# Kernel optimization log

Measured on AMD Instinct MI355X. Metric: run time of the kernel, lower is better.

Reference implementation:

```python
import jax, jax.numpy as jnp
import numpy as np

N_NODES = 100000
N_EDGES = 1600000
INPUT_DIM, HIDDEN_DIM, OUTPUT_DIM = 128, 256, 2
BN_EPS = 1e-5


def setup_inputs() -> dict:
    key = jax.random.key(0)
    ks = jax.random.split(key, 8)
    x = jax.random.normal(ks[0], (N_NODES, INPUT_DIM), jnp.float32)
    edge_index = jax.random.randint(ks[1], (2, N_EDGES), 0, N_NODES, dtype=jnp.int32).astype(jnp.int64)
    # Glorot-ish init for GCNConv weights; PyG GCNConv has bias by default.
    def glorot(k, fan_in, fan_out):
        s = jnp.sqrt(6.0 / (fan_in + fan_out))
        return jax.random.uniform(k, (fan_in, fan_out), jnp.float32, -s, s)
    return {
        "x": x,
        "edge_index": edge_index,
        "W0": glorot(ks[2], INPUT_DIM, HIDDEN_DIM),
        "b0": jnp.zeros((HIDDEN_DIM,), jnp.float32),
        "W1": glorot(ks[3], HIDDEN_DIM, HIDDEN_DIM),
        "b1": jnp.zeros((HIDDEN_DIM,), jnp.float32),
        "W2": glorot(ks[4], HIDDEN_DIM, OUTPUT_DIM),
        "b2": jnp.zeros((OUTPUT_DIM,), jnp.float32),
        "gamma0": jnp.ones((HIDDEN_DIM,), jnp.float32),
        "beta0": jnp.zeros((HIDDEN_DIM,), jnp.float32),
        "gamma1": jnp.ones((HIDDEN_DIM,), jnp.float32),
        "beta1": jnp.zeros((HIDDEN_DIM,), jnp.float32),
    }


def _gcn_norm(edge_index, num_nodes):
    # PyG gcn_norm: add self-loops, deg over destination, D^-1/2 A_hat D^-1/2
    loop = jnp.arange(num_nodes, dtype=edge_index.dtype)
    src = jnp.concatenate([edge_index[0], loop])
    dst = jnp.concatenate([edge_index[1], loop])
    deg = jax.ops.segment_sum(jnp.ones_like(dst, jnp.float32), dst, num_segments=num_nodes)
    dinv = jax.lax.rsqrt(jnp.maximum(deg, 1.0))  # deg >= 1 due to self-loops
    norm = dinv[src] * dinv[dst]  # [E + N]
    return src, dst, norm


def _gcn_conv(x, W, b, src, dst, norm, num_nodes):
    h = x @ W                          # [N, out] dense GEMM first (PyG order)
    msg = h[src] * norm[:, None]       # gather + edge scale
    out = jax.ops.segment_sum(msg, dst, num_segments=num_nodes)  # scatter-add
    return out + b


def _batchnorm(x, gamma, beta):
    # training-mode BatchNorm1d over nodes (biased variance, as torch uses for normalization)
    mean = jnp.mean(x, axis=0)
    var = jnp.mean(jnp.square(x - mean), axis=0)
    return (x - mean) * jax.lax.rsqrt(var + BN_EPS) * gamma + beta


def reference(x, edge_index, W0, b0, W1, b1, W2, b2, gamma0, beta0, gamma1, beta1):
    n = x.shape[0]
    src, dst, norm = _gcn_norm(edge_index, n)
    h = _gcn_conv(x, W0, b0, src, dst, norm, n)
    h = jax.nn.relu(_batchnorm(h, gamma0, beta0))  # dropout is identity (eval / deterministic)
    h = _gcn_conv(h, W1, b1, src, dst, norm, n)
    h = jax.nn.relu(_batchnorm(h, gamma1, beta1))
    out = _gcn_conv(h, W2, b2, src, dst, norm, n)
    return out
```

## Files before the change

### kernel.cpp

```cpp
#include <hip/hip_runtime.h>
#include <hip/hip_fp16.h>


#define BN_EPS 1e-5f

union HF4 { float4 f; __half2 h[4]; };

typedef __attribute__((ext_vector_type(8))) _Float16 f16x8;
typedef __attribute__((ext_vector_type(4))) float f32x4;

__global__ void detect_i64(const unsigned int* __restrict__ w, int* flag) {
  __shared__ unsigned int red[256];
  unsigned int v = 0;
  int t = threadIdx.x;
  for (int i = t; i < 1024; i += 256) v |= w[2 * i + 1];
  red[t] = v;
  __syncthreads();
  for (int s = 128; s > 0; s >>= 1) {
    if (t < s) red[t] |= red[t + s];
    __syncthreads();
  }
  if (t == 0) *flag = (red[0] == 0u) ? 1 : 0;
}

__global__ void convert_deg(const unsigned int* __restrict__ w, const int* __restrict__ flag,
                            int* __restrict__ srcI, int* __restrict__ dstI,
                            int* __restrict__ deg, int E) {
  int i = blockIdx.x * blockDim.x + threadIdx.x;
  if (i >= E) return;
  int f = *flag;
  int s = (int)(f ? w[2 * (size_t)i] : w[i]);
  int d = (int)(f ? w[2 * ((size_t)E + i)] : w[(size_t)E + i]);
  srcI[i] = s;
  dstI[i] = d;
  atomicAdd(&deg[d], 1);
}

__global__ void make_dinv(const int* __restrict__ deg, float* __restrict__ dinv,
                          float* __restrict__ stats, int N) {
  int i = blockIdx.x * blockDim.x + threadIdx.x;
  if (i < 512) stats[i] = 0.f;
  if (i < N) dinv[i] = rsqrtf((float)deg[i] + 1.0f);
}

__global__ void scan_partial(const int* __restrict__ deg, int* __restrict__ blksum, int N) {
  __shared__ int s[256];
  int b = blockIdx.x, t = threadIdx.x;
  int base = b * 1024 + t * 4;
  int v = 0;
#pragma unroll
  for (int k = 0; k < 4; ++k) {
    int i = base + k;
    if (i < N) v += deg[i];
  }
  s[t] = v;
  __syncthreads();
  for (int st = 128; st > 0; st >>= 1) {
    if (t < st) s[t] += s[t + st];
    __syncthreads();
  }
  if (t == 0) blksum[b] = s[0];
}

__global__ void scan_blk(int* __restrict__ blksum, int B) {
  __shared__ int s[256];
  int t = threadIdx.x;
  int v = (t < B) ? blksum[t] : 0;
  s[t] = v;
  __syncthreads();
  for (int off = 1; off < 256; off <<= 1) {
    int u = (t >= off) ? s[t - off] : 0;
    __syncthreads();
    s[t] += u;
    __syncthreads();
  }
  if (t < B) blksum[t] = s[t] - v;
}

__global__ void scan_final(const int* __restrict__ deg, const int* __restrict__ blkoff,
                           int* __restrict__ rowptr, int* __restrict__ fill, int N, int E) {
  __shared__ int s[256];
  int b = blockIdx.x, t = threadIdx.x;
  int base = b * 1024 + t * 4;
  int v[4];
  int sum = 0;
#pragma unroll
  for (int k = 0; k < 4; ++k) {
    int i = base + k;
    v[k] = (i < N) ? deg[i] : 0;
    sum += v[k];
  }
  s[t] = sum;
  __syncthreads();
  for (int off = 1; off < 256; off <<= 1) {
    int u = (t >= off) ? s[t - off] : 0;
    __syncthreads();
    s[t] += u;
    __syncthreads();
  }
  int ex = s[t] - sum + blkoff[b];
#pragma unroll
  for (int k = 0; k < 4; ++k) {
    int i = base + k;
    if (i < N) {
      rowptr[i] = ex;
      fill[i] = ex;
      ex += v[k];
    }
  }
  if (b == 0 && t == 0) rowptr[N] = E;
}

__global__ void csr_scatter(const int* __restrict__ src, const int* __restrict__ dst,
                            const float* __restrict__ dinv, int* __restrict__ fill,
                            int2* __restrict__ edge, int E) {
  int e = blockIdx.x * blockDim.x + threadIdx.x;
  if (e >= E) return;
  int s = src[e], d = dst[e];
  int slot = atomicAdd(&fill[d], 1);
  edge[slot] = make_int2(s, __float_as_int(dinv[s] * dinv[d]));
}

__global__ void f32_to_f16(const float4* __restrict__ in, float4* __restrict__ outh, long n8) {
  long t = (long)blockIdx.x * blockDim.x + threadIdx.x;
  if (t >= n8) return;
  float4 a = in[2 * t], b = in[2 * t + 1];
  HF4 o;
  o.h[0] = __floats2half2_rn(a.x, a.y);
  o.h[1] = __floats2half2_rn(a.z, a.w);
  o.h[2] = __floats2half2_rn(b.x, b.y);
  o.h[3] = __floats2half2_rn(b.z, b.w);
  outh[t] = o.f;
}

__global__ void pack_w2(const float* __restrict__ W0, const float* __restrict__ W1,
                        _Float16* __restrict__ W0p, _Float16* __restrict__ W1p) {
  int idx = blockIdx.x * blockDim.x + threadIdx.x;
  const float* W = (idx < 128 * 256) ? W0 : W1;
  _Float16* Wp = (idx < 128 * 256) ? W0p : W1p;
  int li = (idx < 128 * 256) ? idx : idx - 128 * 256;
  int k = li >> 8, n = li & 255;
  int kb = k >> 5, kk = k & 31, seg = kk >> 3, j = kk & 7;
  Wp[(((kb * 4 + seg) * 256) + n) * 8 + j] = (_Float16)W[li];
}

template <int LPN, bool BN>
__global__ void agg_gather_h(const float4* __restrict__ inh, float4* __restrict__ outh,
                             const int* __restrict__ rowptr, const int2* __restrict__ edge,
                             const float* __restrict__ dinv,
                             const float* __restrict__ scale, const float* __restrict__ shift,
                             int N) {
  long g = (long)blockIdx.x * blockDim.x + threadIdx.x;
  int n = (int)(g / LPN);
  int lane = (int)(g & (LPN - 1));
  if (n >= N) return;
  float sc[8], sh[8];
  if (BN) {
    int c0 = lane * 8;
#pragma unroll
    for (int i = 0; i < 8; ++i) {
      sc[i] = scale[c0 + i];
      sh[i] = shift[c0 + i];
    }
  }
  auto xf = [&](const HF4& u, float* o) {
#pragma unroll
    for (int i = 0; i < 4; ++i) {
      float2 f = __half22float2(u.h[i]);
      o[2 * i] = f.x;
      o[2 * i + 1] = f.y;
    }
    if (BN) {
#pragma unroll
      for (int i = 0; i < 8; ++i) o[i] = fmaxf(o[i] * sc[i] + sh[i], 0.f);
    }
  };
  float ws = dinv[n];
  ws *= ws;
  float acc[8], v[8];
  {
    HF4 u;
    u.f = inh[(long)n * LPN + lane];
    xf(u, v);
#pragma unroll
    for (int i = 0; i < 8; ++i) acc[i] = ws * v[i];
  }
  int beg = rowptr[n], end = rowptr[n + 1];
  int j = beg;
  for (; j + 3 < end; j += 4) {
    int2 e0 = edge[j], e1 = edge[j + 1], e2 = edge[j + 2], e3 = edge[j + 3];
    float w0 = __int_as_float(e0.y), w1 = __int_as_float(e1.y);
    float w2 = __int_as_float(e2.y), w3 = __int_as_float(e3.y);
    HF4 a, b, c, d;
    a.f = inh[(long)e0.x * LPN + lane];
    b.f = inh[(long)e1.x * LPN + lane];
    c.f = inh[(long)e2.x * LPN + lane];
    d.f = inh[(long)e3.x * LPN + lane];
    float va[8], vb[8], vc[8], vd[8];
    xf(a, va); xf(b, vb); xf(c, vc); xf(d, vd);
#pragma unroll
    for (int i = 0; i < 8; ++i)
      acc[i] += w0 * va[i] + w1 * vb[i] + w2 * vc[i] + w3 * vd[i];
  }
  for (; j < end; ++j) {
    int2 e0 = edge[j];
    float w0 = __int_as_float(e0.y);
    HF4 a;
    a.f = inh[(long)e0.x * LPN + lane];
    float va[8];
    xf(a, va);
#pragma unroll
    for (int i = 0; i < 8; ++i) acc[i] += w0 * va[i];
  }
  HF4 o;
  o.h[0] = __floats2half2_rn(acc[0], acc[1]);
  o.h[1] = __floats2half2_rn(acc[2], acc[3]);
  o.h[2] = __floats2half2_rn(acc[4], acc[5]);
  o.h[3] = __floats2half2_rn(acc[6], acc[7]);
  outh[(long)n * LPN + lane] = o.f;
}

template <int K, int NC>
__global__ __launch_bounds__(256) void gemm_mfma(const _Float16* __restrict__ A,
                                                 const float4* __restrict__ Wpack,
                                                 _Float16* __restrict__ H,
                                                 float* __restrict__ gsum,
                                                 float* __restrict__ gsq, int M) {
  __shared__ float red0[NC];
  __shared__ float red1[NC];
  int tid = threadIdx.x;
  if (tid < NC) {
    red0[tid] = 0.f;
    red1[tid] = 0.f;
  }
  __syncthreads();
  int wave = tid >> 6;
  int lane = tid & 63;
  int row0 = (blockIdx.x * 4 + wave) * 32;
  bool active = row0 + 31 < M;
  int arow0 = active ? row0 : 0;
  int r = lane & 15;
  int seg = lane >> 4;
  f32x4 acc0[NC / 16], acc1[NC / 16];
#pragma unroll
  for (int t = 0; t < NC / 16; ++t) {
    acc0[t] = (f32x4){0.f, 0.f, 0.f, 0.f};
    acc1[t] = (f32x4){0.f, 0.f, 0.f, 0.f};
  }
  const _Float16* arowA = A + (long)(arow0 + r) * K;
  const _Float16* arowB = A + (long)(arow0 + 16 + r) * K;
#pragma unroll
  for (int k0 = 0; k0 < K; k0 += 32) {
    f16x8 af0 = *(const f16x8*)(arowA + k0 + seg * 8);
    f16x8 af1 = *(const f16x8*)(arowB + k0 + seg * 8);
    const float4* wp = Wpack + ((k0 >> 5) * 4 + seg) * NC;
#pragma unroll
    for (int t = 0; t < NC / 16; ++t) {
      f16x8 bf = *(const f16x8*)(wp + t * 16 + r);
      acc0[t] = __builtin_amdgcn_mfma_f32_16x16x32_f16(af0, bf, acc0[t], 0, 0, 0);
      acc1[t] = __builtin_amdgcn_mfma_f32_16x16x32_f16(af1, bf, acc1[t], 0, 0, 0);
    }
  }
#pragma unroll
  for (int t = 0; t < NC / 16; ++t) {
    int c = t * 16 + r;
    float s = 0.f, q = 0.f;
#pragma unroll
    for (int qq = 0; qq < 4; ++qq) {
      float v0 = acc0[t][qq], v1 = acc1[t][qq];
      s += v0 + v1;
      q += v0 * v0 + v1 * v1;
    }
    s += __shfl_xor(s, 16, 64);
    s += __shfl_xor(s, 32, 64);
    q += __shfl_xor(q, 16, 64);
    q += __shfl_xor(q, 32, 64);
    if (active) {
      if (seg == 0) {
        atomicAdd(&red0[c], s);
        atomicAdd(&red1[c], q);
      }
#pragma unroll
      for (int qq = 0; qq < 4; ++qq) {
        H[(long)(row0 + seg * 4 + qq) * NC + c] = (_Float16)acc0[t][qq];
        H[(long)(row0 + 16 + seg * 4 + qq) * NC + c] = (_Float16)acc1[t][qq];
      }
    }
  }
  __syncthreads();
  if (tid < NC) {
    atomicAdd(&gsum[tid], red0[tid]);
    atomicAdd(&gsq[tid], red1[tid]);
  }
}

__global__ void bn_finalize(float* __restrict__ gsum, float* __restrict__ gsq,
                            const float* __restrict__ gamma, const float* __restrict__ beta,
                            float* __restrict__ scale, float* __restrict__ shift, float invN) {
  int c = threadIdx.x;
  float mean = gsum[c] * invN;
  float var = fmaxf(gsq[c] * invN - mean * mean, 0.f);
  float sc = rsqrtf(var + BN_EPS) * gamma[c];
  scale[c] = sc;
  shift[c] = beta[c] - mean * sc;
  gsum[c] = 0.f;
  gsq[c] = 0.f;
}

__global__ void bn_apply_proj(const float4* __restrict__ h_in, const float* __restrict__ scale,
                              const float* __restrict__ shift, const float* __restrict__ W2,
                              float* __restrict__ P, int N) {
  int tid = threadIdx.x;
  int row = blockIdx.x * 8 + (tid >> 5);
  int lr = tid & 31;
  if (row >= N) return;
  HF4 u;
  u.f = h_in[(long)row * 32 + lr];
  int c0 = lr * 8;
  float s0 = 0.f, s1 = 0.f;
#pragma unroll
  for (int i = 0; i < 4; ++i) {
    float2 f = __half22float2(u.h[i]);
    int ca = c0 + 2 * i, cb = c0 + 2 * i + 1;
    float va = fmaxf(f.x * scale[ca] + shift[ca], 0.f);
    float vb = fmaxf(f.y * scale[cb] + shift[cb], 0.f);
    s0 += va * W2[2 * ca] + vb * W2[2 * cb];
    s1 += va * W2[2 * ca + 1] + vb * W2[2 * cb + 1];
  }
#pragma unroll
  for (int off = 16; off > 0; off >>= 1) {
    s0 += __shfl_down(s0, off, 32);
    s1 += __shfl_down(s1, off, 32);
  }
  if (lr == 0) {
    P[2 * row] = s0;
    P[2 * row + 1] = s1;
  }
}

__global__ void final_gather(const float* __restrict__ P, float* __restrict__ out,
                             const int* __restrict__ rowptr, const int2* __restrict__ edge,
                             const float* __restrict__ dinv, const float* __restrict__ b2,
                             int N) {
  int n = blockIdx.x * blockDim.x + threadIdx.x;
  if (n >= N) return;
  float w = dinv[n] * dinv[n];
  float a0 = w * P[2 * n + 0];
  float a1 = w * P[2 * n + 1];
  int end = rowptr[n + 1];
  for (int j = rowptr[n]; j < end; ++j) {
    int2 e = edge[j];
    float ww = __int_as_float(e.y);
    a0 += ww * P[2 * e.x + 0];
    a1 += ww * P[2 * e.x + 1];
  }
  out[2 * n + 0] = a0 + b2[0];
  out[2 * n + 1] = a1 + b2[1];
}

extern "C" void kernel_launch(void* const* d_in, const int* in_sizes, int n_in,
                              void* d_out, int out_size, void* d_ws, size_t ws_size,
                              hipStream_t stream) {
  const float* x = (const float*)d_in[0];
  const unsigned int* eidx = (const unsigned int*)d_in[1];
  const float* W0 = (const float*)d_in[2];
  const float* W1 = (const float*)d_in[4];
  const float* W2 = (const float*)d_in[6];
  const float* b2 = (const float*)d_in[7];
  const float* gamma0 = (const float*)d_in[8];
  const float* beta0 = (const float*)d_in[9];
  const float* gamma1 = (const float*)d_in[10];
  const float* beta1 = (const float*)d_in[11];

  const int N = in_sizes[0] / 128;
  const int E = in_sizes[1] / 2;
  float* out = (float*)d_out;

  char* base = (char*)d_ws;
  size_t off = 0;
  auto alloc = [&](size_t bytes) {
    size_t o = off;
    off = (off + bytes + 255) & ~(size_t)255;
    return o;
  };
  const size_t o_edge = alloc((size_t)E * 8);
  const size_t o_rowptr = alloc((size_t)(N + 1) * 4);
  const size_t o_deg = alloc((size_t)N * 4);
  const size_t o_fill = alloc((size_t)N * 4);
  const size_t o_dinv = alloc((size_t)N * 4);
  const size_t o_blk = alloc(1024 * 4);
  const size_t o_flag = alloc(256);
  const size_t o_stats = alloc(4096);
  const size_t o_P = alloc((size_t)N * 2 * 4);
  const size_t o_W0p = alloc(128 * 256 * 2);
  const size_t o_W1p = alloc(256 * 256 * 2);
  const size_t o_H1 = alloc((size_t)N * 256 * 2);
  const size_t o_H2 = alloc((size_t)N * 256 * 2);

  int2* edge = (int2*)(base + o_edge);
  int* rowptr = (int*)(base + o_rowptr);
  int* deg = (int*)(base + o_deg);
  int* fill = (int*)(base + o_fill);
  float* dinv = (float*)(base + o_dinv);
  int* blk = (int*)(base + o_blk);
  int* flag = (int*)(base + o_flag);
  float* gsum = (float*)(base + o_stats);
  float* gsq = gsum + 256;
  float* scale = gsum + 512;
  float* shift = gsum + 768;
  float* P = (float*)(base + o_P);
  _Float16* W0p = (_Float16*)(base + o_W0p);
  _Float16* W1p = (_Float16*)(base + o_W1p);
  float4* H1 = (float4*)(base + o_H1);
  float4* H2 = (float4*)(base + o_H2);
  int* idx32 = (int*)(base + o_H2);
  int* srcI = idx32;
  int* dstI = idx32 + E;

  auto cdiv = [](long a, long b) { return (int)((a + b - 1) / b); };
  const float invN = 1.0f / (float)N;
  const int B1 = cdiv(N, 1024);

  hipLaunchKernelGGL(detect_i64, dim3(1), dim3(256), 0, stream, eidx, flag);
  hipMemsetAsync(deg, 0, (size_t)N * 4, stream);
  hipLaunchKernelGGL(convert_deg, dim3(cdiv(E, 256)), dim3(256), 0, stream, eidx, flag, srcI,
                     dstI, deg, E);

  hipLaunchKernelGGL(make_dinv, dim3(cdiv(N, 256)), dim3(256), 0, stream, deg, dinv, gsum, N);
  hipLaunchKernelGGL(scan_partial, dim3(B1), dim3(256), 0, stream, deg, blk, N);
  hipLaunchKernelGGL(scan_blk, dim3(1), dim3(256), 0, stream, blk, B1);
  hipLaunchKernelGGL(scan_final, dim3(B1), dim3(256), 0, stream, deg, blk, rowptr, fill, N, E);
  hipLaunchKernelGGL(csr_scatter, dim3(cdiv(E, 256)), dim3(256), 0, stream, srcI, dstI, dinv,
                     fill, edge, E);
  hipLaunchKernelGGL(pack_w2, dim3(cdiv(384 * 256, 256)), dim3(256), 0, stream, W0, W1, W0p, W1p);
  hipLaunchKernelGGL(f32_to_f16, dim3(cdiv((long)N * 16, 256)), dim3(256), 0, stream,
                     (const float4*)x, H1, (long)N * 16);

  hipLaunchKernelGGL((agg_gather_h<16, false>), dim3(cdiv((long)N * 16, 256)), dim3(256), 0,
                     stream, H1, H2, rowptr, edge, dinv, nullptr, nullptr, N);
  hipLaunchKernelGGL((gemm_mfma<128, 256>), dim3(cdiv(N, 128)), dim3(256), 0, stream,
                     (const _Float16*)H2, (const float4*)W0p, (_Float16*)H1, gsum, gsq, N);

  hipLaunchKernelGGL(bn_finalize, dim3(1), dim3(256), 0, stream, gsum, gsq, gamma0, beta0, scale,
                     shift, invN);

  hipLaunchKernelGGL((agg_gather_h<32, true>), dim3(cdiv((long)N * 32, 256)), dim3(256), 0,
                     stream, H1, H2, rowptr, edge, dinv, scale, shift, N);
  hipLaunchKernelGGL((gemm_mfma<256, 256>), dim3(cdiv(N, 128)), dim3(256), 0, stream,
                     (const _Float16*)H2, (const float4*)W1p, (_Float16*)H1, gsum, gsq, N);

  hipLaunchKernelGGL(bn_finalize, dim3(1), dim3(256), 0, stream, gsum, gsq, gamma1, beta1, scale,
                     shift, invN);
  hipLaunchKernelGGL(bn_apply_proj, dim3(cdiv(N, 8)), dim3(256), 0, stream, (const float4*)H1,
                     scale, shift, W2, P, N);

  hipLaunchKernelGGL(final_gather, dim3(cdiv(N, 256)), dim3(256), 0, stream, P, out, rowptr,
                     edge, dinv, b2, N);
}
```

Before: 554.1 us.

## Store CSR column indices only, recompute edge weights from dinv; fuse prep kernels

After: 603.4 us. 8.9% more time.

```diff
diff --git a/kernel.cpp b/kernel.cpp
--- a/kernel.cpp
+++ b/kernel.cpp
@@ -27,31 +27,53 @@
                             int* __restrict__ srcI, int* __restrict__ dstI,
                             int* __restrict__ deg, int E) {
   int i = blockIdx.x * blockDim.x + threadIdx.x;
-  if (i >= E) return;
+  int e0 = 2 * i;
+  if (e0 >= E) return;
   int f = *flag;
-  int s = (int)(f ? w[2 * (size_t)i] : w[i]);
-  int d = (int)(f ? w[2 * ((size_t)E + i)] : w[(size_t)E + i]);
-  srcI[i] = s;
-  dstI[i] = d;
-  atomicAdd(&deg[d], 1);
-}
-
-__global__ void make_dinv(const int* __restrict__ deg, float* __restrict__ dinv,
-                          float* __restrict__ stats, int N) {
-  int i = blockIdx.x * blockDim.x + threadIdx.x;
-  if (i < 512) stats[i] = 0.f;
-  if (i < N) dinv[i] = rsqrtf((float)deg[i] + 1.0f);
-}
-
-__global__ void scan_partial(const int* __restrict__ deg, int* __restrict__ blksum, int N) {
+  if (e0 + 1 < E) {
+    int s0, s1, d0, d1;
+    if (f) {
+      uint4 sv = ((const uint4*)w)[i];
+      uint4 dv = ((const uint4*)(w + 2 * (size_t)E))[i];
+      s0 = (int)sv.x; s1 = (int)sv.z;
+      d0 = (int)dv.x; d1 = (int)dv.z;
+    } else {
+      int2 sv = ((const int2*)w)[i];
+      int2 dv = ((const int2*)(w + (size_t)E))[i];
+      s0 = sv.x; s1 = sv.y;
+      d0 = dv.x; d1 = dv.y;
+    }
+    *(int2*)(srcI + e0) = make_int2(s0, s1);
+    *(int2*)(dstI + e0) = make_int2(d0, d1);
+    atomicAdd(&deg[d0], 1);
+    atomicAdd(&deg[d1], 1);
+  } else {
+    int s = (int)(f ? w[2 * (size_t)e0] : w[e0]);
+    int d = (int)(f ? w[2 * ((size_t)E + e0)] : w[(size_t)E + e0]);
+    srcI[e0] = s;
+    dstI[e0] = d;
+    atomicAdd(&deg[d], 1);
+  }
+}
+
+__global__ void scan_partial(const int* __restrict__ deg, int* __restrict__ blksum,
+                             float* __restrict__ dinv, float* __restrict__ stats, int N) {
   __shared__ int s[256];
   int b = blockIdx.x, t = threadIdx.x;
+  if (b == 0) {
+    stats[t] = 0.f;
+    stats[t + 256] = 0.f;
+  }
   int base = b * 1024 + t * 4;
   int v = 0;
 #pragma unroll
   for (int k = 0; k < 4; ++k) {
     int i = base + k;
-    if (i < N) v += deg[i];
+    if (i < N) {
+      int dg = deg[i];
+      v += dg;
+      dinv[i] = rsqrtf((float)dg + 1.0f);
+    }
   }
   s[t] = v;
   __syncthreads();
@@ -112,41 +134,43 @@
 }
 
 __global__ void csr_scatter(const int* __restrict__ src, const int* __restrict__ dst,
-                            const float* __restrict__ dinv, int* __restrict__ fill,
-                            int2* __restrict__ edge, int E) {
+                            int* __restrict__ fill, int* __restrict__ col, int E) {
   int e = blockIdx.x * blockDim.x + threadIdx.x;
   if (e >= E) return;
   int s = src[e], d = dst[e];
   int slot = atomicAdd(&fill[d], 1);
-  edge[slot] = make_int2(s, __float_as_int(dinv[s] * dinv[d]));
-}
-
-__global__ void f32_to_f16(const float4* __restrict__ in, float4* __restrict__ outh, long n8) {
-  long t = (long)blockIdx.x * blockDim.x + threadIdx.x;
-  if (t >= n8) return;
-  float4 a = in[2 * t], b = in[2 * t + 1];
-  HF4 o;
-  o.h[0] = __floats2half2_rn(a.x, a.y);
-  o.h[1] = __floats2half2_rn(a.z, a.w);
-  o.h[2] = __floats2half2_rn(b.x, b.y);
-  o.h[3] = __floats2half2_rn(b.z, b.w);
-  outh[t] = o.f;
-}
-
-__global__ void pack_w2(const float* __restrict__ W0, const float* __restrict__ W1,
-                        _Float16* __restrict__ W0p, _Float16* __restrict__ W1p) {
-  int idx = blockIdx.x * blockDim.x + threadIdx.x;
-  const float* W = (idx < 128 * 256) ? W0 : W1;
-  _Float16* Wp = (idx < 128 * 256) ? W0p : W1p;
-  int li = (idx < 128 * 256) ? idx : idx - 128 * 256;
-  int k = li >> 8, n = li & 255;
-  int kb = k >> 5, kk = k & 31, seg = kk >> 3, j = kk & 7;
-  Wp[(((kb * 4 + seg) * 256) + n) * 8 + j] = (_Float16)W[li];
+  col[slot] = s;
+}
+
+__global__ void prep_pack_convert(const float* __restrict__ W0, const float* __restrict__ W1,
+                                  _Float16* __restrict__ W0p, _Float16* __restrict__ W1p,
+                                  const float4* __restrict__ x, float4* __restrict__ xh,
+                                  long n8) {
+  long b = blockIdx.x;
+  if (b < 384) {
+    int idx = (int)b * 256 + threadIdx.x;
+    const float* W = (idx < 128 * 256) ? W0 : W1;
+    _Float16* Wp = (idx < 128 * 256) ? W0p : W1p;
+    int li = (idx < 128 * 256) ? idx : idx - 128 * 256;
+    int k = li >> 8, n = li & 255;
+    int kb = k >> 5, kk = k & 31, seg = kk >> 3, j = kk & 7;
+    Wp[(((kb * 4 + seg) * 256) + n) * 8 + j] = (_Float16)W[li];
+  } else {
+    long t = (b - 384) * 256 + threadIdx.x;
+    if (t >= n8) return;
+    float4 a = x[2 * t], c = x[2 * t + 1];
+    HF4 o;
+    o.h[0] = __floats2half2_rn(a.x, a.y);
+    o.h[1] = __floats2half2_rn(a.z, a.w);
+    o.h[2] = __floats2half2_rn(c.x, c.y);
+    o.h[3] = __floats2half2_rn(c.z, c.w);
+    xh[t] = o.f;
+  }
 }
 
 template <int LPN, bool BN>
 __global__ void agg_gather_h(const float4* __restrict__ inh, float4* __restrict__ outh,
-                             const int* __restrict__ rowptr, const int2* __restrict__ edge,
+                             const int* __restrict__ rowptr, const int* __restrict__ col,
                              const float* __restrict__ dinv,
                              const float* __restrict__ scale, const float* __restrict__ shift,
                              int N) {
@@ -175,8 +199,8 @@
       for (int i = 0; i < 8; ++i) o[i] = fmaxf(o[i] * sc[i] + sh[i], 0.f);
     }
   };
-  float ws = dinv[n];
-  ws *= ws;
+  float dn = dinv[n];
+  float ws = dn * dn;
   float acc[8], v[8];
   {
     HF4 u;
@@ -188,14 +212,14 @@
   int beg = rowptr[n], end = rowptr[n + 1];
   int j = beg;
   for (; j + 3 < end; j += 4) {
-    int2 e0 = edge[j], e1 = edge[j + 1], e2 = edge[j + 2], e3 = edge[j + 3];
-    float w0 = __int_as_float(e0.y), w1 = __int_as_float(e1.y);
-    float w2 = __int_as_float(e2.y), w3 = __int_as_float(e3.y);
+    int c0 = col[j], c1 = col[j + 1], c2 = col[j + 2], c3 = col[j + 3];
+    float w0 = dinv[c0] * dn, w1 = dinv[c1] * dn;
+    float w2 = dinv[c2] * dn, w3 = dinv[c3] * dn;
     HF4 a, b, c, d;
-    a.f = inh[(long)e0.x * LPN + lane];
-    b.f = inh[(long)e1.x * LPN + lane];
-    c.f = inh[(long)e2.x * LPN + lane];
-    d.f = inh[(long)e3.x * LPN + lane];
+    a.f = inh[(long)c0 * LPN + lane];
+    b.f = inh[(long)c1 * LPN + lane];
+    c.f = inh[(long)c2 * LPN + lane];
+    d.f = inh[(long)c3 * LPN + lane];
     float va[8], vb[8], vc[8], vd[8];
     xf(a, va); xf(b, vb); xf(c, vc); xf(d, vd);
 #pragma unroll
@@ -203,10 +227,10 @@
       acc[i] += w0 * va[i] + w1 * vb[i] + w2 * vc[i] + w3 * vd[i];
   }
   for (; j < end; ++j) {
-    int2 e0 = edge[j];
-    float w0 = __int_as_float(e0.y);
+    int c0 = col[j];
+    float w0 = dinv[c0] * dn;
     HF4 a;
-    a.f = inh[(long)e0.x * LPN + lane];
+    a.f = inh[(long)c0 * LPN + lane];
     float va[8];
     xf(a, va);
 #pragma unroll
@@ -339,20 +363,21 @@
 }
 
 __global__ void final_gather(const float* __restrict__ P, float* __restrict__ out,
-                             const int* __restrict__ rowptr, const int2* __restrict__ edge,
+                             const int* __restrict__ rowptr, const int* __restrict__ col,
                              const float* __restrict__ dinv, const float* __restrict__ b2,
                              int N) {
   int n = blockIdx.x * blockDim.x + threadIdx.x;
   if (n >= N) return;
-  float w = dinv[n] * dinv[n];
+  float dn = dinv[n];
+  float w = dn * dn;
   float a0 = w * P[2 * n + 0];
   float a1 = w * P[2 * n + 1];
   int end = rowptr[n + 1];
   for (int j = rowptr[n]; j < end; ++j) {
-    int2 e = edge[j];
-    float ww = __int_as_float(e.y);
-    a0 += ww * P[2 * e.x + 0];
-    a1 += ww * P[2 * e.x + 1];
+    int c = col[j];
+    float ww = dinv[c] * dn;
+    a0 += ww * P[2 * c + 0];
+    a1 += ww * P[2 * c + 1];
   }
   out[2 * n + 0] = a0 + b2[0];
   out[2 * n + 1] = a1 + b2[1];
@@ -383,7 +408,7 @@
     off = (off + bytes + 255) & ~(size_t)255;
     return o;
   };
-  const size_t o_edge = alloc((size_t)E * 8);
+  const size_t o_col = alloc((size_t)E * 4);
   const size_t o_rowptr = alloc((size_t)(N + 1) * 4);
   const size_t o_deg = alloc((size_t)N * 4);
   const size_t o_fill = alloc((size_t)N * 4);
@@ -397,7 +422,7 @@
   const size_t o_H1 = alloc((size_t)N * 256 * 2);
   const size_t o_H2 = alloc((size_t)N * 256 * 2);
 
-  int2* edge = (int2*)(base + o_edge);
+  int* col = (int*)(base + o_col);
   int* rowptr = (int*)(base + o_rowptr);
   int* deg = (int*)(base + o_deg);
   int* fill = (int*)(base + o_fill);
@@ -423,21 +448,19 @@
 
   hipLaunchKernelGGL(detect_i64, dim3(1), dim3(256), 0, stream, eidx, flag);
   hipMemsetAsync(deg, 0, (size_t)N * 4, stream);
-  hipLaunchKernelGGL(convert_deg, dim3(cdiv(E, 256)), dim3(256), 0, stream, eidx, flag, srcI,
-                     dstI, deg, E);
-
-  hipLaunchKernelGGL(make_dinv, dim3(cdiv(N, 256)), dim3(256), 0, stream, deg, dinv, gsum, N);
-  hipLaunchKernelGGL(scan_partial, dim3(B1), dim3(256), 0, stream, deg, blk, N);
+  hipLaunchKernelGGL(convert_deg, dim3(cdiv(cdiv(E, 2), 256)), dim3(256), 0, stream, eidx, flag,
+                     srcI, dstI, deg, E);
+
+  hipLaunchKernelGGL(scan_partial, dim3(B1), dim3(256), 0, stream, deg, blk, dinv, gsum, N);
   hipLaunchKernelGGL(scan_blk, dim3(1), dim3(256), 0, stream, blk, B1);
   hipLaunchKernelGGL(scan_final, dim3(B1), dim3(256), 0, stream, deg, blk, rowptr, fill, N, E);
-  hipLaunchKernelGGL(csr_scatter, dim3(cdiv(E, 256)), dim3(256), 0, stream, srcI, dstI, dinv,
-                     fill, edge, E);
-  hipLaunchKernelGGL(pack_w2, dim3(cdiv(384 * 256, 256)), dim3(256), 0, stream, W0, W1, W0p, W1p);
-  hipLaunchKernelGGL(f32_to_f16, dim3(cdiv((long)N * 16, 256)), dim3(256), 0, stream,
-                     (const float4*)x, H1, (long)N * 16);
+  hipLaunchKernelGGL(csr_scatter, dim3(cdiv(E, 256)), dim3(256), 0, stream, srcI, dstI, fill,
+                     col, E);
+  hipLaunchKernelGGL(prep_pack_convert, dim3(384 + cdiv((long)N * 16, 256)), dim3(256), 0,
+                     stream, W0, W1, W0p, W1p, (const float4*)x, H1, (long)N * 16);
 
   hipLaunchKernelGGL((agg_gather_h<16, false>), dim3(cdiv((long)N * 16, 256)), dim3(256), 0,
-                     stream, H1, H2, rowptr, edge, dinv, nullptr, nullptr, N);
+                     stream, H1, H2, rowptr, col, dinv, nullptr, nullptr, N);
   hipLaunchKernelGGL((gemm_mfma<128, 256>), dim3(cdiv(N, 128)), dim3(256), 0, stream,
                      (const _Float16*)H2, (const float4*)W0p, (_Float16*)H1, gsum, gsq, N);
 
@@ -445,7 +468,7 @@
                      shift, invN);
 
   hipLaunchKernelGGL((agg_gather_h<32, true>), dim3(cdiv((long)N * 32, 256)), dim3(256), 0,
-                     stream, H1, H2, rowptr, edge, dinv, scale, shift, N);
+                     stream, H1, H2, rowptr, col, dinv, scale, shift, N);
   hipLaunchKernelGGL((gemm_mfma<256, 256>), dim3(cdiv(N, 128)), dim3(256), 0, stream,
                      (const _Float16*)H2, (const float4*)W1p, (_Float16*)H1, gsum, gsq, N);
 
@@ -454,6 +477,6 @@
   hipLaunchKernelGGL(bn_apply_proj, dim3(cdiv(N, 8)), dim3(256), 0, stream, (const float4*)H1,
                      scale, shift, W2, P, N);
 
-  hipLaunchKernelGGL(final_gather, dim3(cdiv(N, 256)), dim3(256), 0, stream, P, out, rowptr,
-                     edge, dinv, b2, N);
-}
+  hipLaunchKernelGGL(final_gather, dim3(cdiv(N, 256)), dim3(256), 0, stream, P, out, rowptr, col,
+                     dinv, b2, N);
+}
```
